# Kernel tuning notes

Measured on AMD Instinct MI355X. Metric: run time of the kernel, lower is better.

## Reference

```python
import jax, jax.numpy as jnp
import numpy as np

N_NODES = 10000
N_EDGES = 640000
STATE_DIM = 128
ACTION_DIM = 10000
K = 3  # Chebyshev order
H1, H2, H3 = 60, 30, 1
CONCAT_DIM = N_NODES + 3  # 10003


def setup_inputs() -> dict:
    key = jax.random.key(0)
    ks = jax.random.split(key, 16)
    inp = {
        "substrate_features": jax.random.normal(ks[0], (N_NODES, STATE_DIM), jnp.float32),
        "edge_index": jax.random.randint(ks[1], (2, N_EDGES), 0, N_NODES, jnp.int64),
        "v_CPU_request": jax.random.uniform(ks[2], (1,), jnp.float32),
        "v_BW_demand": jax.random.uniform(ks[3], (1,), jnp.float32),
        "pending_v_nodes": jax.random.uniform(ks[4], (1,), jnp.float32),
        # ChebConv weights: [K, in, out] (PyG stores one Linear per hop)
        "W1": jax.random.normal(ks[5], (K, STATE_DIM, H1), jnp.float32) / np.sqrt(STATE_DIM),
        "b1": jnp.zeros((H1,), jnp.float32),
        "W2": jax.random.normal(ks[6], (K, H1, H2), jnp.float32) / np.sqrt(H1),
        "b2": jnp.zeros((H2,), jnp.float32),
        "W3": jax.random.normal(ks[7], (K, H2, H3), jnp.float32) / np.sqrt(H2),
        "b3": jnp.zeros((H3,), jnp.float32),
        # actor / critic heads
        "Wa": jax.random.normal(ks[8], (ACTION_DIM, CONCAT_DIM), jnp.float32) / np.sqrt(CONCAT_DIM),
        "ba": jnp.zeros((ACTION_DIM,), jnp.float32),
        "Wc": jax.random.normal(ks[9], (1, CONCAT_DIM), jnp.float32) / np.sqrt(CONCAT_DIM),
        "bc": jnp.zeros((1,), jnp.float32),
    }
    return inp


def _edge_norm(edge_index, n_nodes):
    # PyG ChebConv sym normalization with lambda_max=2: L_hat = -D^-1/2 A D^-1/2 (diag = 0)
    src, dst = edge_index[0], edge_index[1]
    deg = jax.ops.segment_sum(jnp.ones_like(src, jnp.float32), dst, num_segments=n_nodes)
    dinv = jnp.where(deg > 0, 1.0 / jnp.sqrt(deg), 0.0)
    w = -dinv[src] * dinv[dst]  # [E]
    return src, dst, w


def _lap_matvec(x, src, dst, w, n_nodes):
    # y[i] = sum_{e: dst[e]=i} w[e] * x[src[e]]
    return jax.ops.segment_sum(w[:, None] * x[src], dst, num_segments=n_nodes)


def _cheb_conv(x, src, dst, w, n_nodes, W, b):
    # T0 = x; T1 = L_hat x; T2 = 2 L_hat T1 - T0
    Tx0 = x
    out = Tx0 @ W[0]
    Tx1 = _lap_matvec(Tx0, src, dst, w, n_nodes)
    out = out + Tx1 @ W[1]
    for k in range(2, W.shape[0]):
        Tx2 = 2.0 * _lap_matvec(Tx1, src, dst, w, n_nodes) - Tx0
        out = out + Tx2 @ W[k]
        Tx0, Tx1 = Tx1, Tx2
    return out + b


def reference(substrate_features, edge_index, v_CPU_request, v_BW_demand,
              pending_v_nodes, W1, b1, W2, b2, W3, b3, Wa, ba, Wc, bc):
    n = substrate_features.shape[0]
    src, dst, w = _edge_norm(edge_index, n)
    h = jnp.tanh(_cheb_conv(substrate_features, src, dst, w, n, W1, b1))
    h = jnp.tanh(_cheb_conv(h, src, dst, w, n, W2, b2))
    h = jnp.tanh(_cheb_conv(h, src, dst, w, n, W3, b3))  # [N, 1]
    gcn_embedding = h.reshape(1, n)  # squeeze last dim -> row vector [1, N]
    state = jnp.concatenate(
        [gcn_embedding, v_CPU_request[None, :], v_BW_demand[None, :],
         pending_v_nodes[None, :]], axis=1)  # [1, N+3]
    logits = state @ Wa.T + ba   # [1, action_dim]
    values = state @ Wc.T + bc   # [1, 1]
    return logits, values
```

## Files before the change

kernel.cpp:

```cpp
#include <hip/hip_runtime.h>
#include <hip/hip_bf16.h>

#define NN 10000
#define NE 640000
#define SD 128
#define CONCAT 10003
#define ACT 10000
#define MAXDEG 256
#define GB 2500
#define HB 2512

typedef unsigned int u32;
typedef unsigned short u16;
typedef u16 u16x8 __attribute__((ext_vector_type(8)));
typedef float f32x4 __attribute__((ext_vector_type(4)));

__device__ __forceinline__ float bf2f_bits(u16 u) {
    return __uint_as_float(((u32)u) << 16);
}
__device__ __forceinline__ float loadF(const void* base, long idx, int bf) {
    if (bf) return bf2f_bits(((const u16*)base)[idx]);
    return ((const float*)base)[idx];
}
__device__ __forceinline__ int loadI(const void* base, long idx, int i64) {
    if (i64) return (int)((const long long*)base)[idx];
    return ((const int*)base)[idx];
}

__global__ void __launch_bounds__(256) k_prep(
    const void* __restrict__ x_in, const void* __restrict__ W1,
    const void* __restrict__ Wa, const void* __restrict__ edge,
    int* __restrict__ flags, int* __restrict__ cnt,
    float* __restrict__ P0, float* __restrict__ P1, float* __restrict__ P2) {
    __shared__ int sbf;
    const int tid = threadIdx.x, gid = blockIdx.x;
    const int gtid = gid * 256 + tid;
    const int lane = tid & 63;
    const int wid = gid * 4 + (tid >> 6);

    if (tid == 0) {
        const u32* w = (const u32*)Wa;
        int c = 0;
        for (int j = 0; j < 256; ++j) {
            u32 lo = w[j] & 0xFFFFu;
            int ex = (int)((lo >> 7) & 0xFF);
            if (ex >= 100 && ex <= 140) c++;
        }
        sbf = (c >= 128) ? 1 : 0;
        if (gid == 0) {
            const int* e32 = (const int*)edge;
            int cnt64 = 0;
            for (int e = 0; e < 64; ++e) {
                int lo = e32[2 * e], hi = e32[2 * e + 1];
                if (hi == 0 && lo >= 0 && lo < NN) cnt64++;
            }
            flags[0] = (cnt64 >= 56) ? 1 : 0;
            flags[1] = sbf;
        }
    }
    __syncthreads();
    const int bf = sbf;

    for (int i = gtid; i < NN; i += GB * 256) cnt[i] = 0;

    int o = lane < 60 ? lane : 59;
    for (int r = wid; r < NN; r += GB * 4) {
        float xa, xb;
        if (bf) {
            u32 wbits = ((const u32*)x_in)[(long)r * 64 + lane];
            xa = bf2f_bits((u16)(wbits & 0xFFFFu));
            xb = bf2f_bits((u16)(wbits >> 16));
        } else {
            const float* xp = (const float*)x_in + (long)r * SD + 2 * lane;
            xa = xp[0];
            xb = xp[1];
        }
        float a0 = 0.f, a1 = 0.f, a2 = 0.f;
        for (int j2 = 0; j2 < 64; ++j2) {
            float xe = __shfl(xa, j2);
            float xo = __shfl(xb, j2);
            long je = (long)(2 * j2) * 60 + o;
            long jo = (long)(2 * j2 + 1) * 60 + o;
            a0 += xe * loadF(W1, 0 * SD * 60 + je, bf) + xo * loadF(W1, 0 * SD * 60 + jo, bf);
            a1 += xe * loadF(W1, 1 * SD * 60 + je, bf) + xo * loadF(W1, 1 * SD * 60 + jo, bf);
            a2 += xe * loadF(W1, 2 * SD * 60 + je, bf) + xo * loadF(W1, 2 * SD * 60 + jo, bf);
        }
        if (lane < 60) {
            P0[(long)r * 60 + lane] = a0;
            P1[(long)r * 60 + lane] = a1;
            P2[(long)r * 60 + lane] = a2;
        }
    }
}

__global__ void __launch_bounds__(256) k_fill(
    const void* __restrict__ edge, const int* __restrict__ flags,
    int* __restrict__ cnt, int* __restrict__ cols) {
    const int i64f = flags[0];
    int e = blockIdx.x * 256 + threadIdx.x;
    for (; e < NE; e += GB * 256) {
        int s = loadI(edge, e, i64f);
        int d = loadI(edge, NE + e, i64f);
        int pos = atomicAdd(&cnt[d], 1);
        if (pos < MAXDEG) cols[(size_t)d * MAXDEG + pos] = s;
    }
}

__global__ void __launch_bounds__(256) k_s1(
    const int* __restrict__ cnt, const int* __restrict__ cols,
    float* __restrict__ wve, const float* __restrict__ P1,
    const float* __restrict__ P2, float* __restrict__ W60) {
    const int tid = threadIdx.x;
    const int lane = tid & 63;
    const int wid = blockIdx.x * 4 + (tid >> 6);
    int o = lane < 60 ? lane : 59;
    for (int r = wid; r < NN; r += GB * 4) {
        int cr = cnt[r];
        if (cr > MAXDEG) cr = MAXDEG;
        float rr = cr > 0 ? rsqrtf((float)cr) : 0.f;
        const int* cp = cols + (size_t)r * MAXDEG;
        float* wp = wve + (size_t)r * MAXDEG;
        float acc = 0.f;
        int p = 0;
        for (; p + 3 < cr; p += 4) {
            int s0 = cp[p], s1 = cp[p + 1], s2 = cp[p + 2], s3 = cp[p + 3];
            int c0 = cnt[s0], c1 = cnt[s1], c2 = cnt[s2], c3 = cnt[s3];
            float w0 = c0 > 0 ? -rsqrtf((float)c0) * rr : 0.f;
            float w1 = c1 > 0 ? -rsqrtf((float)c1) * rr : 0.f;
            float w2 = c2 > 0 ? -rsqrtf((float)c2) * rr : 0.f;
            float w3 = c3 > 0 ? -rsqrtf((float)c3) * rr : 0.f;
            acc += w0 * P2[(size_t)s0 * 60 + o] + w1 * P2[(size_t)s1 * 60 + o] +
                   w2 * P2[(size_t)s2 * 60 + o] + w3 * P2[(size_t)s3 * 60 + o];
            if (lane == 63) {
                wp[p] = w0;
                wp[p + 1] = w1;
                wp[p + 2] = w2;
                wp[p + 3] = w3;
            }
        }
        for (; p < cr; ++p) {
            int s = cp[p];
            int cs = cnt[s];
            float w = cs > 0 ? -rsqrtf((float)cs) * rr : 0.f;
            acc += w * P2[(size_t)s * 60 + o];
            if (lane == 63) wp[p] = w;
        }
        if (lane < 60)
            W60[(size_t)r * 60 + lane] = P1[(size_t)r * 60 + lane] + 2.f * acc;
    }
}

__global__ void __launch_bounds__(256) k_s2(
    const int* __restrict__ cnt, const int* __restrict__ cols,
    const float* __restrict__ wve, const float* __restrict__ P0,
    const float* __restrict__ P2, const float* __restrict__ W60,
    const void* __restrict__ W2, const void* __restrict__ b1,
    const int* __restrict__ flags, float* __restrict__ Q0,
    float* __restrict__ Q1, float* __restrict__ Q2) {
    const int bf = flags[1];
    const int tid = threadIdx.x;
    const int lane = tid & 63;
    const int wid = blockIdx.x * 4 + (tid >> 6);
    int o = lane < 60 ? lane : 59;
    int o2 = lane < 30 ? lane : 29;
    for (int r = wid; r < NN; r += GB * 4) {
        int cr = cnt[r];
        if (cr > MAXDEG) cr = MAXDEG;
        const int* cp = cols + (size_t)r * MAXDEG;
        const float* wp = wve + (size_t)r * MAXDEG;
        float acc = 0.f;
        int p = 0;
        for (; p + 3 < cr; p += 4) {
            acc += wp[p] * W60[(size_t)cp[p] * 60 + o] +
                   wp[p + 1] * W60[(size_t)cp[p + 1] * 60 + o] +
                   wp[p + 2] * W60[(size_t)cp[p + 2] * 60 + o] +
                   wp[p + 3] * W60[(size_t)cp[p + 3] * 60 + o];
        }
        for (; p < cr; ++p) acc += wp[p] * W60[(size_t)cp[p] * 60 + o];
        float h1 = tanhf(P0[(size_t)r * 60 + o] - P2[(size_t)r * 60 + o] + acc +
                         loadF(b1, o, bf));
        float q0 = 0.f, q1 = 0.f, q2 = 0.f;
        for (int j = 0; j < 60; ++j) {
            float xj = __shfl(h1, j);
            long idx = (long)j * 30 + o2;
            q0 += xj * loadF(W2, 0 * 60 * 30 + idx, bf);
            q1 += xj * loadF(W2, 1 * 60 * 30 + idx, bf);
            q2 += xj * loadF(W2, 2 * 60 * 30 + idx, bf);
        }
        if (lane < 30) {
            Q0[(size_t)r * 30 + lane] = q0;
            Q1[(size_t)r * 30 + lane] = q1;
            Q2[(size_t)r * 30 + lane] = q2;
        }
    }
}

__global__ void __launch_bounds__(256) k_s3(
    const int* __restrict__ cnt, const int* __restrict__ cols,
    const float* __restrict__ wve, const float* __restrict__ Q1,
    const float* __restrict__ Q2, float* __restrict__ W30) {
    const int tid = threadIdx.x;
    const int lane = tid & 63;
    const int wid = blockIdx.x * 4 + (tid >> 6);
    int h = lane >> 5, l = lane & 31;
    int l2 = l < 30 ? l : 29;
    for (int r = wid; r < NN; r += GB * 4) {
        int cr = cnt[r];
        if (cr > MAXDEG) cr = MAXDEG;
        const int* cp = cols + (size_t)r * MAXDEG;
        const float* wp = wve + (size_t)r * MAXDEG;
        float acc = 0.f;
        for (int p = h; p < cr; p += 2) acc += wp[p] * Q2[(size_t)cp[p] * 30 + l2];
        acc += __shfl_xor(acc, 32);
        if (lane < 30)
            W30[(size_t)r * 30 + lane] = Q1[(size_t)r * 30 + lane] + 2.f * acc;
    }
}

__global__ void __launch_bounds__(256) k_s4(
    const int* __restrict__ cnt, const int* __restrict__ cols,
    const float* __restrict__ wve, const float* __restrict__ Q0,
    const float* __restrict__ Q2, const float* __restrict__ W30,
    const void* __restrict__ W3, const void* __restrict__ b2,
    const int* __restrict__ flags, float* __restrict__ R1,
    float* __restrict__ R2, float* __restrict__ Sa) {
    const int bf = flags[1];
    const int tid = threadIdx.x;
    const int lane = tid & 63;
    const int wid = blockIdx.x * 4 + (tid >> 6);
    int h = lane >> 5, l = lane & 31;
    int l2 = l < 30 ? l : 29;
    for (int r = wid; r < NN; r += GB * 4) {
        int cr = cnt[r];
        if (cr > MAXDEG) cr = MAXDEG;
        const int* cp = cols + (size_t)r * MAXDEG;
        const float* wp = wve + (size_t)r * MAXDEG;
        float acc = 0.f;
        for (int p = h; p < cr; p += 2) acc += wp[p] * W30[(size_t)cp[p] * 30 + l2];
        acc += __shfl_xor(acc, 32);
        float r0 = 0.f, r1 = 0.f, r2 = 0.f;
        if (l < 30) {
            float h2v = tanhf(Q0[(size_t)r * 30 + l] - Q2[(size_t)r * 30 + l] + acc +
                              loadF(b2, l, bf));
            r0 = h2v * loadF(W3, 0 * 30 + l, bf);
            r1 = h2v * loadF(W3, 1 * 30 + l, bf);
            r2 = h2v * loadF(W3, 2 * 30 + l, bf);
        }
#pragma unroll
        for (int m = 16; m; m >>= 1) {
            r0 += __shfl_xor(r0, m);
            r1 += __shfl_xor(r1, m);
            r2 += __shfl_xor(r2, m);
        }
        if (lane == 0) {
            R1[r] = r1;
            R2[r] = r2;
            Sa[r] = r0 - r2;
        }
    }
}

__global__ void __launch_bounds__(256) k_s5(
    const int* __restrict__ cnt, const int* __restrict__ cols,
    const float* __restrict__ wve, const float* __restrict__ R1,
    const float* __restrict__ R2, float* __restrict__ Wv3) {
    const int tid = threadIdx.x;
    const int lane = tid & 63;
    const int wid = blockIdx.x * 4 + (tid >> 6);
    for (int r = wid; r < NN; r += GB * 4) {
        int cr = cnt[r];
        if (cr > MAXDEG) cr = MAXDEG;
        const int* cp = cols + (size_t)r * MAXDEG;
        const float* wp = wve + (size_t)r * MAXDEG;
        float acc = 0.f;
        for (int p = lane; p < cr; p += 64) acc += wp[p] * R2[cp[p]];
#pragma unroll
        for (int m = 32; m; m >>= 1) acc += __shfl_xor(acc, m);
        if (lane == 0) Wv3[r] = R1[r] + 2.f * acc;
    }
}

__global__ void __launch_bounds__(256) k_s6(
    const int* __restrict__ cnt, const int* __restrict__ cols,
    const float* __restrict__ wve, const float* __restrict__ Sa,
    const float* __restrict__ Wv3, const void* __restrict__ b3,
    const void* sc0, const void* sc1, const void* sc2,
    const int* __restrict__ flags, float* __restrict__ state) {
    const int bf = flags[1];
    const int tid = threadIdx.x;
    const int lane = tid & 63;
    const int wid = blockIdx.x * 4 + (tid >> 6);
    for (int r = wid; r < NN; r += GB * 4) {
        int cr = cnt[r];
        if (cr > MAXDEG) cr = MAXDEG;
        const int* cp = cols + (size_t)r * MAXDEG;
        const float* wp = wve + (size_t)r * MAXDEG;
        float acc = 0.f;
        for (int p = lane; p < cr; p += 64) acc += wp[p] * Wv3[cp[p]];
#pragma unroll
        for (int m = 32; m; m >>= 1) acc += __shfl_xor(acc, m);
        if (lane == 0) state[r] = tanhf(Sa[r] + acc + loadF(b3, 0, bf));
    }
    if (blockIdx.x == 0 && tid == 0) {
        state[10000] = loadF(sc0, 0, bf);
        state[10001] = loadF(sc1, 0, bf);
        state[10002] = loadF(sc2, 0, bf);
    }
}

__global__ void __launch_bounds__(256) k_heads(
    const float* __restrict__ state, const void* __restrict__ Wa,
    const void* __restrict__ ba, const void* __restrict__ Wc,
    const void* __restrict__ bc, const int* __restrict__ flags,
    void* __restrict__ out) {
    const int bf = flags[1];
    const int tid = threadIdx.x;
    const int lane = tid & 63;
    const int wid = blockIdx.x * 4 + (tid >> 6);
    for (int r = wid; r <= ACT; r += HB * 4) {
        long base = (r < ACT) ? (long)r * CONCAT : 0;
        const void* wb = (r < ACT) ? Wa : Wc;
        float acc = 0.f;
        if (bf) {
            const u16* w = (const u16*)wb + base;
            int k = (int)((16 - ((2 * base) & 15)) & 15) >> 1;
            for (int i = lane; i < k; i += 64) acc += state[i] * bf2f_bits(w[i]);
            int nv = (CONCAT - k) >> 3;
            const u16x8* wvp = (const u16x8*)(w + k);
            for (int v = lane; v < nv; v += 64) {
                u16x8 ww = wvp[v];
                int ib = k + v * 8;
#pragma unroll
                for (int j = 0; j < 8; ++j) acc += state[ib + j] * bf2f_bits(ww[j]);
            }
            for (int i = k + nv * 8 + lane; i < CONCAT; i += 64)
                acc += state[i] * bf2f_bits(w[i]);
        } else {
            const float* w = (const float*)wb + base;
            int k = (int)((16 - ((4 * base) & 15)) & 15) >> 2;
            for (int i = lane; i < k; i += 64) acc += state[i] * w[i];
            int nv = (CONCAT - k) >> 2;
            const f32x4* wvp = (const f32x4*)(w + k);
            for (int v = lane; v < nv; v += 64) {
                f32x4 ww = wvp[v];
                int ib = k + v * 4;
#pragma unroll
                for (int j = 0; j < 4; ++j) acc += state[ib + j] * ww[j];
            }
            for (int i = k + nv * 4 + lane; i < CONCAT; i += 64)
                acc += state[i] * w[i];
        }
#pragma unroll
        for (int o = 32; o > 0; o >>= 1) acc += __shfl_xor(acc, o);
        if (lane == 0) {
            float bias = (r < ACT) ? loadF(ba, r, bf) : loadF(bc, 0, bf);
            float v = acc + bias;
            if (bf) ((__hip_bfloat16*)out)[r] = __float2bfloat16(v);
            else ((float*)out)[r] = v;
        }
    }
}

extern "C" void kernel_launch(void* const* d_in, const int* in_sizes, int n_in,
                              void* d_out, int out_size, void* d_ws, size_t ws_size,
                              hipStream_t stream) {
    const void* x_in = d_in[0];
    const void* edge = d_in[1];
    const void* sc0 = d_in[2];
    const void* sc1 = d_in[3];
    const void* sc2 = d_in[4];
    const void* W1 = d_in[5];
    const void* b1 = d_in[6];
    const void* W2 = d_in[7];
    const void* b2 = d_in[8];
    const void* W3 = d_in[9];
    const void* b3 = d_in[10];
    const void* Wa = d_in[11];
    const void* ba = d_in[12];
    const void* Wc = d_in[13];
    const void* bc = d_in[14];

    char* p = (char*)d_ws;
    auto alloc = [&](size_t bytes) {
        char* r = p;
        p += (bytes + 255) & ~(size_t)255;
        return (void*)r;
    };
    int* flags = (int*)alloc(2 * 4);
    int* cnt = (int*)alloc(NN * 4);
    int* cols = (int*)alloc((size_t)NN * MAXDEG * 4);
    float* wve = (float*)alloc((size_t)NN * MAXDEG * 4);
    float* P0 = (float*)alloc((size_t)NN * 60 * 4);
    float* P1 = (float*)alloc((size_t)NN * 60 * 4);
    float* P2 = (float*)alloc((size_t)NN * 60 * 4);
    float* W60 = (float*)alloc((size_t)NN * 60 * 4);
    float* Q0 = (float*)alloc((size_t)NN * 30 * 4);
    float* Q1 = (float*)alloc((size_t)NN * 30 * 4);
    float* Q2 = (float*)alloc((size_t)NN * 30 * 4);
    float* W30 = (float*)alloc((size_t)NN * 30 * 4);
    float* R1 = (float*)alloc(NN * 4);
    float* R2 = (float*)alloc(NN * 4);
    float* Sa = (float*)alloc(NN * 4);
    float* Wv3 = (float*)alloc(NN * 4);
    float* state = (float*)alloc(CONCAT * 4);

    k_prep<<<GB, 256, 0, stream>>>(x_in, W1, Wa, edge, flags, cnt, P0, P1, P2);
    k_fill<<<GB, 256, 0, stream>>>(edge, flags, cnt, cols);
    k_s1<<<GB, 256, 0, stream>>>(cnt, cols, wve, P1, P2, W60);
    k_s2<<<GB, 256, 0, stream>>>(cnt, cols, wve, P0, P2, W60, W2, b1, flags, Q0, Q1, Q2);
    k_s3<<<GB, 256, 0, stream>>>(cnt, cols, wve, Q1, Q2, W30);
    k_s4<<<GB, 256, 0, stream>>>(cnt, cols, wve, Q0, Q2, W30, W3, b2, flags, R1, R2, Sa);
    k_s5<<<GB, 256, 0, stream>>>(cnt, cols, wve, R1, R2, Wv3);
    k_s6<<<GB, 256, 0, stream>>>(cnt, cols, wve, Sa, Wv3, b3, sc0, sc1, sc2, flags, state);
    k_heads<<<HB, 256, 0, stream>>>(state, Wa, ba, Wc, bc, flags, d_out);
}
```

Measured before the change: 351.9 us.

## Fuse prep and fill kernels via grid barrier; fuse last two hop kernels

Merges the feature projection and CSR fill kernels into one launch of 1024 blocks. A software grid barrier separates zeroing the counters from the atomic fill; it uses per-block flags that the heads kernel resets for the next call. Also fuses the final two sparse matvecs into one kernel that recomputes each neighbor's inner sum redundantly, a two-hop gather costing roughly degree-squared work per row. This removes two launches and a global intermediate, but relies on all 1024 blocks being co-resident, and the recomputation may dominate.

```diff
diff --git a/kernel.cpp b/kernel.cpp
--- a/kernel.cpp
+++ b/kernel.cpp
@@ -7,8 +7,10 @@
 #define CONCAT 10003
 #define ACT 10000
 #define MAXDEG 256
+#define GB1 1024
 #define GB 2500
 #define HB 2512
+#define MAGIC 0x5A17C0DE
 
 typedef unsigned int u32;
 typedef unsigned short u16;
@@ -27,18 +29,27 @@
     return ((const int*)base)[idx];
 }
 
-__global__ void __launch_bounds__(256) k_prep(
+__global__ void __launch_bounds__(256, 4) k_prep_fill(
     const void* __restrict__ x_in, const void* __restrict__ W1,
     const void* __restrict__ Wa, const void* __restrict__ edge,
-    int* __restrict__ flags, int* __restrict__ cnt,
-    float* __restrict__ P0, float* __restrict__ P1, float* __restrict__ P2) {
-    __shared__ int sbf;
+    int* __restrict__ flags, int* __restrict__ cnt, int* __restrict__ cols,
+    float* __restrict__ P0, float* __restrict__ P1, float* __restrict__ P2,
+    int* bar, int* bargo) {
+    __shared__ int sflags[2];
+    __shared__ int sdone;
     const int tid = threadIdx.x, gid = blockIdx.x;
     const int gtid = gid * 256 + tid;
     const int lane = tid & 63;
     const int wid = gid * 4 + (tid >> 6);
 
     if (tid == 0) {
+        const int* e32 = (const int*)edge;
+        int cnt64 = 0;
+        for (int e = 0; e < 64; ++e) {
+            int lo = e32[2 * e], hi = e32[2 * e + 1];
+            if (hi == 0 && lo >= 0 && lo < NN) cnt64++;
+        }
+        sflags[0] = (cnt64 >= 56) ? 1 : 0;
         const u32* w = (const u32*)Wa;
         int c = 0;
         for (int j = 0; j < 256; ++j) {
@@ -46,62 +57,82 @@
             int ex = (int)((lo >> 7) & 0xFF);
             if (ex >= 100 && ex <= 140) c++;
         }
-        sbf = (c >= 128) ? 1 : 0;
+        sflags[1] = (c >= 128) ? 1 : 0;
         if (gid == 0) {
-            const int* e32 = (const int*)edge;
-            int cnt64 = 0;
-            for (int e = 0; e < 64; ++e) {
-                int lo = e32[2 * e], hi = e32[2 * e + 1];
-                if (hi == 0 && lo >= 0 && lo < NN) cnt64++;
-            }
-            flags[0] = (cnt64 >= 56) ? 1 : 0;
-            flags[1] = sbf;
+            flags[0] = sflags[0];
+            flags[1] = sflags[1];
         }
     }
     __syncthreads();
-    const int bf = sbf;
-
-    for (int i = gtid; i < NN; i += GB * 256) cnt[i] = 0;
-
-    int o = lane < 60 ? lane : 59;
-    for (int r = wid; r < NN; r += GB * 4) {
-        float xa, xb;
-        if (bf) {
-            u32 wbits = ((const u32*)x_in)[(long)r * 64 + lane];
-            xa = bf2f_bits((u16)(wbits & 0xFFFFu));
-            xb = bf2f_bits((u16)(wbits >> 16));
-        } else {
-            const float* xp = (const float*)x_in + (long)r * SD + 2 * lane;
-            xa = xp[0];
-            xb = xp[1];
-        }
-        float a0 = 0.f, a1 = 0.f, a2 = 0.f;
-        for (int j2 = 0; j2 < 64; ++j2) {
-            float xe = __shfl(xa, j2);
-            float xo = __shfl(xb, j2);
-            long je = (long)(2 * j2) * 60 + o;
-            long jo = (long)(2 * j2 + 1) * 60 + o;
-            a0 += xe * loadF(W1, 0 * SD * 60 + je, bf) + xo * loadF(W1, 0 * SD * 60 + jo, bf);
-            a1 += xe * loadF(W1, 1 * SD * 60 + je, bf) + xo * loadF(W1, 1 * SD * 60 + jo, bf);
-            a2 += xe * loadF(W1, 2 * SD * 60 + je, bf) + xo * loadF(W1, 2 * SD * 60 + jo, bf);
-        }
-        if (lane < 60) {
-            P0[(long)r * 60 + lane] = a0;
-            P1[(long)r * 60 + lane] = a1;
-            P2[(long)r * 60 + lane] = a2;
-        }
-    }
-}
-
-__global__ void __launch_bounds__(256) k_fill(
-    const void* __restrict__ edge, const int* __restrict__ flags,
-    int* __restrict__ cnt, int* __restrict__ cols) {
-    const int i64f = flags[0];
-    int e = blockIdx.x * 256 + threadIdx.x;
-    for (; e < NE; e += GB * 256) {
+    const int i64f = sflags[0], bf = sflags[1];
+
+    for (int i = gtid; i < NN; i += GB1 * 256)
+        __hip_atomic_store(&cnt[i], 0, __ATOMIC_RELAXED, __HIP_MEMORY_SCOPE_AGENT);
+
+    {
+        int o = lane < 60 ? lane : 59;
+        for (int r = wid; r < NN; r += GB1 * 4) {
+            float xa, xb;
+            if (bf) {
+                u32 wbits = ((const u32*)x_in)[(long)r * 64 + lane];
+                xa = bf2f_bits((u16)(wbits & 0xFFFFu));
+                xb = bf2f_bits((u16)(wbits >> 16));
+            } else {
+                const float* xp = (const float*)x_in + (long)r * SD + 2 * lane;
+                xa = xp[0];
+                xb = xp[1];
+            }
+            float a0 = 0.f, a1 = 0.f, a2 = 0.f;
+            for (int j2 = 0; j2 < 64; ++j2) {
+                float xe = __shfl(xa, j2);
+                float xo = __shfl(xb, j2);
+                long je = (long)(2 * j2) * 60 + o;
+                long jo = (long)(2 * j2 + 1) * 60 + o;
+                a0 += xe * loadF(W1, 0 * SD * 60 + je, bf) + xo * loadF(W1, 0 * SD * 60 + jo, bf);
+                a1 += xe * loadF(W1, 1 * SD * 60 + je, bf) + xo * loadF(W1, 1 * SD * 60 + jo, bf);
+                a2 += xe * loadF(W1, 2 * SD * 60 + je, bf) + xo * loadF(W1, 2 * SD * 60 + jo, bf);
+            }
+            if (lane < 60) {
+                P0[(long)r * 60 + lane] = a0;
+                P1[(long)r * 60 + lane] = a1;
+                P2[(long)r * 60 + lane] = a2;
+            }
+        }
+    }
+
+    asm volatile("s_waitcnt vmcnt(0)" ::: "memory");
+    __syncthreads();
+    if (tid == 0)
+        __hip_atomic_store(&bar[gid], MAGIC, __ATOMIC_RELAXED, __HIP_MEMORY_SCOPE_AGENT);
+    if (gid == 0) {
+        int it = 0;
+        while (true) {
+            if (tid == 0) sdone = 1;
+            __syncthreads();
+            int ok = 1;
+            for (int b = tid; b < GB1; b += 256)
+                if (__hip_atomic_load(&bar[b], __ATOMIC_RELAXED, __HIP_MEMORY_SCOPE_AGENT) != MAGIC)
+                    ok = 0;
+            if (!ok) sdone = 0;
+            __syncthreads();
+            if (sdone != 0 || ++it > (1 << 22)) break;
+            __builtin_amdgcn_s_sleep(4);
+        }
+        if (tid == 0)
+            __hip_atomic_store(bargo, MAGIC, __ATOMIC_RELAXED, __HIP_MEMORY_SCOPE_AGENT);
+    } else if (tid == 0) {
+        int it = 0;
+        while (__hip_atomic_load(bargo, __ATOMIC_RELAXED, __HIP_MEMORY_SCOPE_AGENT) != MAGIC) {
+            if (++it > (1 << 22)) break;
+            __builtin_amdgcn_s_sleep(8);
+        }
+    }
+    __syncthreads();
+
+    for (int e = gtid; e < NE; e += GB1 * 256) {
         int s = loadI(edge, e, i64f);
         int d = loadI(edge, NE + e, i64f);
-        int pos = atomicAdd(&cnt[d], 1);
+        int pos = __hip_atomic_fetch_add(&cnt[d], 1, __ATOMIC_RELAXED, __HIP_MEMORY_SCOPE_AGENT);
         if (pos < MAXDEG) cols[(size_t)d * MAXDEG + pos] = s;
     }
 }
@@ -260,10 +291,13 @@
     }
 }
 
-__global__ void __launch_bounds__(256) k_s5(
+__global__ void __launch_bounds__(256) k_s56(
     const int* __restrict__ cnt, const int* __restrict__ cols,
-    const float* __restrict__ wve, const float* __restrict__ R1,
-    const float* __restrict__ R2, float* __restrict__ Wv3) {
+    const float* __restrict__ wve, const float* __restrict__ Sa,
+    const float* __restrict__ R1, const float* __restrict__ R2,
+    const void* __restrict__ b3, const void* sc0, const void* sc1,
+    const void* sc2, const int* __restrict__ flags, float* __restrict__ state) {
+    const int bf = flags[1];
     const int tid = threadIdx.x;
     const int lane = tid & 63;
     const int wid = blockIdx.x * 4 + (tid >> 6);
@@ -273,30 +307,22 @@
         const int* cp = cols + (size_t)r * MAXDEG;
         const float* wp = wve + (size_t)r * MAXDEG;
         float acc = 0.f;
-        for (int p = lane; p < cr; p += 64) acc += wp[p] * R2[cp[p]];
-#pragma unroll
-        for (int m = 32; m; m >>= 1) acc += __shfl_xor(acc, m);
-        if (lane == 0) Wv3[r] = R1[r] + 2.f * acc;
-    }
-}
-
-__global__ void __launch_bounds__(256) k_s6(
-    const int* __restrict__ cnt, const int* __restrict__ cols,
-    const float* __restrict__ wve, const float* __restrict__ Sa,
-    const float* __restrict__ Wv3, const void* __restrict__ b3,
-    const void* sc0, const void* sc1, const void* sc2,
-    const int* __restrict__ flags, float* __restrict__ state) {
-    const int bf = flags[1];
-    const int tid = threadIdx.x;
-    const int lane = tid & 63;
-    const int wid = blockIdx.x * 4 + (tid >> 6);
-    for (int r = wid; r < NN; r += GB * 4) {
-        int cr = cnt[r];
-        if (cr > MAXDEG) cr = MAXDEG;
-        const int* cp = cols + (size_t)r * MAXDEG;
-        const float* wp = wve + (size_t)r * MAXDEG;
-        float acc = 0.f;
-        for (int p = lane; p < cr; p += 64) acc += wp[p] * Wv3[cp[p]];
+        for (int p = lane; p < cr; p += 64) {
+            int s = cp[p];
+            float w = wp[p];
+            int cs = cnt[s];
+            if (cs > MAXDEG) cs = MAXDEG;
+            const int* cps = cols + (size_t)s * MAXDEG;
+            const float* wps = wve + (size_t)s * MAXDEG;
+            float inner = 0.f;
+            int t = 0;
+            for (; t + 3 < cs; t += 4) {
+                inner += wps[t] * R2[cps[t]] + wps[t + 1] * R2[cps[t + 1]] +
+                         wps[t + 2] * R2[cps[t + 2]] + wps[t + 3] * R2[cps[t + 3]];
+            }
+            for (; t < cs; ++t) inner += wps[t] * R2[cps[t]];
+            acc += w * (R1[s] + 2.f * inner);
+        }
 #pragma unroll
         for (int m = 32; m; m >>= 1) acc += __shfl_xor(acc, m);
         if (lane == 0) state[r] = tanhf(Sa[r] + acc + loadF(b3, 0, bf));
@@ -312,11 +338,15 @@
     const float* __restrict__ state, const void* __restrict__ Wa,
     const void* __restrict__ ba, const void* __restrict__ Wc,
     const void* __restrict__ bc, const int* __restrict__ flags,
-    void* __restrict__ out) {
+    int* bar, int* bargo, void* __restrict__ out) {
     const int bf = flags[1];
     const int tid = threadIdx.x;
     const int lane = tid & 63;
     const int wid = blockIdx.x * 4 + (tid >> 6);
+    if (tid == 0 && blockIdx.x < GB1)
+        __hip_atomic_store(&bar[blockIdx.x], 0, __ATOMIC_RELAXED, __HIP_MEMORY_SCOPE_AGENT);
+    if (tid == 0 && blockIdx.x == GB1)
+        __hip_atomic_store(bargo, 0, __ATOMIC_RELAXED, __HIP_MEMORY_SCOPE_AGENT);
     for (int r = wid; r <= ACT; r += HB * 4) {
         long base = (r < ACT) ? (long)r * CONCAT : 0;
         const void* wb = (r < ACT) ? Wa : Wc;
@@ -387,6 +417,8 @@
         return (void*)r;
     };
     int* flags = (int*)alloc(2 * 4);
+    int* bar = (int*)alloc(GB1 * 4);
+    int* bargo = (int*)alloc(4);
     int* cnt = (int*)alloc(NN * 4);
     int* cols = (int*)alloc((size_t)NN * MAXDEG * 4);
     float* wve = (float*)alloc((size_t)NN * MAXDEG * 4);
@@ -401,16 +433,14 @@
     float* R1 = (float*)alloc(NN * 4);
     float* R2 = (float*)alloc(NN * 4);
     float* Sa = (float*)alloc(NN * 4);
-    float* Wv3 = (float*)alloc(NN * 4);
     float* state = (float*)alloc(CONCAT * 4);
 
-    k_prep<<<GB, 256, 0, stream>>>(x_in, W1, Wa, edge, flags, cnt, P0, P1, P2);
-    k_fill<<<GB, 256, 0, stream>>>(edge, flags, cnt, cols);
+    k_prep_fill<<<GB1, 256, 0, stream>>>(x_in, W1, Wa, edge, flags, cnt, cols,
+                                         P0, P1, P2, bar, bargo);
     k_s1<<<GB, 256, 0, stream>>>(cnt, cols, wve, P1, P2, W60);
     k_s2<<<GB, 256, 0, stream>>>(cnt, cols, wve, P0, P2, W60, W2, b1, flags, Q0, Q1, Q2);
     k_s3<<<GB, 256, 0, stream>>>(cnt, cols, wve, Q1, Q2, W30);
     k_s4<<<GB, 256, 0, stream>>>(cnt, cols, wve, Q0, Q2, W30, W3, b2, flags, R1, R2, Sa);
-    k_s5<<<GB, 256, 0, stream>>>(cnt, cols, wve, R1, R2, Wv3);
-    k_s6<<<GB, 256, 0, stream>>>(cnt, cols, wve, Sa, Wv3, b3, sc0, sc1, sc2, flags, state);
-    k_heads<<<HB, 256, 0, stream>>>(state, Wa, ba, Wc, bc, flags, d_out);
-}
+    k_s56<<<GB, 256, 0, stream>>>(cnt, cols, wve, Sa, R1, R2, b3, sc0, sc1, sc2, flags, state);
+    k_heads<<<HB, 256, 0, stream>>>(state, Wa, ba, Wc, bc, flags, bar, bargo, d_out);
+}
```

Measured after the change: 556.4 us. 1.58x slower.

## Fuse final three Chebyshev stages into one kernel with per-node flag spin-waits

Applied to the files above, without the earlier changes.

Merges the last three sparse stages (k_s4, k_s5, k_s6) into a single kernel of 1024 blocks, each handling a chunk of 10 rows. Intermediate per-row values R1 and Sa stay in registers. R2 and Wv3 are published as 64-bit words tagged with a magic value, and consumers spin on those words instead of waiting for kernel boundaries. This removes two launches and their global-memory round trips. In exchange it relies on all blocks being co-resident, doubles the bytes of each gathered value, and adds atomic polling. The tagged buffers are reset at the end inside k_heads so the next call starts clean.

```diff
diff --git a/kernel.cpp b/kernel.cpp
--- a/kernel.cpp
+++ b/kernel.cpp
@@ -8,10 +8,14 @@
 #define ACT 10000
 #define MAXDEG 256
 #define GB 2500
+#define GB456 1024
+#define CH456 10
 #define HB 2512
+#define MAGIC64 0x5A17C0DEull
 
 typedef unsigned int u32;
 typedef unsigned short u16;
+typedef unsigned long long u64;
 typedef u16 u16x8 __attribute__((ext_vector_type(8)));
 typedef float f32x4 __attribute__((ext_vector_type(4)));
 
@@ -25,6 +29,21 @@
 __device__ __forceinline__ int loadI(const void* base, long idx, int i64) {
     if (i64) return (int)((const long long*)base)[idx];
     return ((const int*)base)[idx];
+}
+__device__ __forceinline__ float spin_load(const u64* p) {
+    u64 v;
+    int it = 0;
+    while (true) {
+        v = __hip_atomic_load(p, __ATOMIC_RELAXED, __HIP_MEMORY_SCOPE_AGENT);
+        if ((v >> 32) == MAGIC64) break;
+        if (++it > (1 << 22)) break;
+        __builtin_amdgcn_s_sleep(1);
+    }
+    return __uint_as_float((u32)v);
+}
+__device__ __forceinline__ void publish(u64* p, float x) {
+    u64 v = (MAGIC64 << 32) | (u64)__float_as_uint(x);
+    __hip_atomic_store(p, v, __ATOMIC_RELAXED, __HIP_MEMORY_SCOPE_AGENT);
 }
 
 __global__ void __launch_bounds__(256) k_prep(
@@ -217,89 +236,96 @@
     }
 }
 
-__global__ void __launch_bounds__(256) k_s4(
+__global__ void __launch_bounds__(256, 4) k_s456(
     const int* __restrict__ cnt, const int* __restrict__ cols,
     const float* __restrict__ wve, const float* __restrict__ Q0,
     const float* __restrict__ Q2, const float* __restrict__ W30,
     const void* __restrict__ W3, const void* __restrict__ b2,
-    const int* __restrict__ flags, float* __restrict__ R1,
-    float* __restrict__ R2, float* __restrict__ Sa) {
+    const void* __restrict__ b3, const void* sc0, const void* sc1,
+    const void* sc2, const int* __restrict__ flags,
+    u64* __restrict__ R2pack, u64* __restrict__ Wv3pack,
+    float* __restrict__ state) {
     const int bf = flags[1];
     const int tid = threadIdx.x;
     const int lane = tid & 63;
-    const int wid = blockIdx.x * 4 + (tid >> 6);
-    int h = lane >> 5, l = lane & 31;
-    int l2 = l < 30 ? l : 29;
-    for (int r = wid; r < NN; r += GB * 4) {
-        int cr = cnt[r];
-        if (cr > MAXDEG) cr = MAXDEG;
-        const int* cp = cols + (size_t)r * MAXDEG;
-        const float* wp = wve + (size_t)r * MAXDEG;
-        float acc = 0.f;
-        for (int p = h; p < cr; p += 2) acc += wp[p] * W30[(size_t)cp[p] * 30 + l2];
-        acc += __shfl_xor(acc, 32);
-        float r0 = 0.f, r1 = 0.f, r2 = 0.f;
-        if (l < 30) {
-            float h2v = tanhf(Q0[(size_t)r * 30 + l] - Q2[(size_t)r * 30 + l] + acc +
-                              loadF(b2, l, bf));
-            r0 = h2v * loadF(W3, 0 * 30 + l, bf);
-            r1 = h2v * loadF(W3, 1 * 30 + l, bf);
-            r2 = h2v * loadF(W3, 2 * 30 + l, bf);
-        }
-#pragma unroll
-        for (int m = 16; m; m >>= 1) {
-            r0 += __shfl_xor(r0, m);
-            r1 += __shfl_xor(r1, m);
-            r2 += __shfl_xor(r2, m);
-        }
-        if (lane == 0) {
-            R1[r] = r1;
-            R2[r] = r2;
-            Sa[r] = r0 - r2;
-        }
-    }
-}
-
-__global__ void __launch_bounds__(256) k_s5(
-    const int* __restrict__ cnt, const int* __restrict__ cols,
-    const float* __restrict__ wve, const float* __restrict__ R1,
-    const float* __restrict__ R2, float* __restrict__ Wv3) {
-    const int tid = threadIdx.x;
-    const int lane = tid & 63;
-    const int wid = blockIdx.x * 4 + (tid >> 6);
-    for (int r = wid; r < NN; r += GB * 4) {
-        int cr = cnt[r];
-        if (cr > MAXDEG) cr = MAXDEG;
-        const int* cp = cols + (size_t)r * MAXDEG;
-        const float* wp = wve + (size_t)r * MAXDEG;
-        float acc = 0.f;
-        for (int p = lane; p < cr; p += 64) acc += wp[p] * R2[cp[p]];
-#pragma unroll
-        for (int m = 32; m; m >>= 1) acc += __shfl_xor(acc, m);
-        if (lane == 0) Wv3[r] = R1[r] + 2.f * acc;
-    }
-}
-
-__global__ void __launch_bounds__(256) k_s6(
-    const int* __restrict__ cnt, const int* __restrict__ cols,
-    const float* __restrict__ wve, const float* __restrict__ Sa,
-    const float* __restrict__ Wv3, const void* __restrict__ b3,
-    const void* sc0, const void* sc1, const void* sc2,
-    const int* __restrict__ flags, float* __restrict__ state) {
-    const int bf = flags[1];
-    const int tid = threadIdx.x;
-    const int lane = tid & 63;
-    const int wid = blockIdx.x * 4 + (tid >> 6);
-    for (int r = wid; r < NN; r += GB * 4) {
-        int cr = cnt[r];
-        if (cr > MAXDEG) cr = MAXDEG;
-        const int* cp = cols + (size_t)r * MAXDEG;
-        const float* wp = wve + (size_t)r * MAXDEG;
-        float acc = 0.f;
-        for (int p = lane; p < cr; p += 64) acc += wp[p] * Wv3[cp[p]];
-#pragma unroll
-        for (int m = 32; m; m >>= 1) acc += __shfl_xor(acc, m);
-        if (lane == 0) state[r] = tanhf(Sa[r] + acc + loadF(b3, 0, bf));
+    const int wslot = tid >> 6;
+    const int rbase = blockIdx.x * CH456;
+
+    float R1reg[3], SAreg[3];
+
+    {
+        int h = lane >> 5, l = lane & 31;
+        int l2 = l < 30 ? l : 29;
+        int k = 0;
+        for (int i = wslot; i < CH456; i += 4, ++k) {
+            int r = rbase + i;
+            if (r >= NN) break;
+            int cr = cnt[r];
+            if (cr > MAXDEG) cr = MAXDEG;
+            const int* cp = cols + (size_t)r * MAXDEG;
+            const float* wp = wve + (size_t)r * MAXDEG;
+            float acc = 0.f;
+            for (int p = h; p < cr; p += 2) acc += wp[p] * W30[(size_t)cp[p] * 30 + l2];
+            acc += __shfl_xor(acc, 32);
+            float r0 = 0.f, r1 = 0.f, r2 = 0.f;
+            if (l < 30) {
+                float h2v = tanhf(Q0[(size_t)r * 30 + l] - Q2[(size_t)r * 30 + l] + acc +
+                                  loadF(b2, l, bf));
+                r0 = h2v * loadF(W3, 0 * 30 + l, bf);
+                r1 = h2v * loadF(W3, 1 * 30 + l, bf);
+                r2 = h2v * loadF(W3, 2 * 30 + l, bf);
+            }
+#pragma unroll
+            for (int m = 16; m; m >>= 1) {
+                r0 += __shfl_xor(r0, m);
+                r1 += __shfl_xor(r1, m);
+                r2 += __shfl_xor(r2, m);
+            }
+            r0 += __shfl_xor(r0, 32);
+            r1 += __shfl_xor(r1, 32);
+            r2 += __shfl_xor(r2, 32);
+            r0 *= 0.5f;
+            r1 *= 0.5f;
+            r2 *= 0.5f;
+            R1reg[k] = r1;
+            SAreg[k] = r0 - r2;
+            if (lane == 0) publish(&R2pack[r], r2);
+        }
+    }
+
+    {
+        int k = 0;
+        for (int i = wslot; i < CH456; i += 4, ++k) {
+            int r = rbase + i;
+            if (r >= NN) break;
+            int cr = cnt[r];
+            if (cr > MAXDEG) cr = MAXDEG;
+            const int* cp = cols + (size_t)r * MAXDEG;
+            const float* wp = wve + (size_t)r * MAXDEG;
+            float acc = 0.f;
+            for (int p = lane; p < cr; p += 64) acc += wp[p] * spin_load(&R2pack[cp[p]]);
+#pragma unroll
+            for (int m = 32; m; m >>= 1) acc += __shfl_xor(acc, m);
+            float wv3 = R1reg[k] + 2.f * acc;
+            if (lane == 0) publish(&Wv3pack[r], wv3);
+        }
+    }
+
+    {
+        int k = 0;
+        for (int i = wslot; i < CH456; i += 4, ++k) {
+            int r = rbase + i;
+            if (r >= NN) break;
+            int cr = cnt[r];
+            if (cr > MAXDEG) cr = MAXDEG;
+            const int* cp = cols + (size_t)r * MAXDEG;
+            const float* wp = wve + (size_t)r * MAXDEG;
+            float acc = 0.f;
+            for (int p = lane; p < cr; p += 64) acc += wp[p] * spin_load(&Wv3pack[cp[p]]);
+#pragma unroll
+            for (int m = 32; m; m >>= 1) acc += __shfl_xor(acc, m);
+            if (lane == 0) state[r] = tanhf(SAreg[k] + acc + loadF(b3, 0, bf));
+        }
     }
     if (blockIdx.x == 0 && tid == 0) {
         state[10000] = loadF(sc0, 0, bf);
@@ -312,11 +338,16 @@
     const float* __restrict__ state, const void* __restrict__ Wa,
     const void* __restrict__ ba, const void* __restrict__ Wc,
     const void* __restrict__ bc, const int* __restrict__ flags,
+    u64* __restrict__ R2pack, u64* __restrict__ Wv3pack,
     void* __restrict__ out) {
     const int bf = flags[1];
     const int tid = threadIdx.x;
     const int lane = tid & 63;
     const int wid = blockIdx.x * 4 + (tid >> 6);
+    for (int i = blockIdx.x * 256 + tid; i < NN; i += HB * 256) {
+        R2pack[i] = 0ull;
+        Wv3pack[i] = 0ull;
+    }
     for (int r = wid; r <= ACT; r += HB * 4) {
         long base = (r < ACT) ? (long)r * CONCAT : 0;
         const void* wb = (r < ACT) ? Wa : Wc;
@@ -398,10 +429,8 @@
     float* Q1 = (float*)alloc((size_t)NN * 30 * 4);
     float* Q2 = (float*)alloc((size_t)NN * 30 * 4);
     float* W30 = (float*)alloc((size_t)NN * 30 * 4);
-    float* R1 = (float*)alloc(NN * 4);
-    float* R2 = (float*)alloc(NN * 4);
-    float* Sa = (float*)alloc(NN * 4);
-    float* Wv3 = (float*)alloc(NN * 4);
+    u64* R2pack = (u64*)alloc((size_t)NN * 8);
+    u64* Wv3pack = (u64*)alloc((size_t)NN * 8);
     float* state = (float*)alloc(CONCAT * 4);
 
     k_prep<<<GB, 256, 0, stream>>>(x_in, W1, Wa, edge, flags, cnt, P0, P1, P2);
@@ -409,8 +438,7 @@
     k_s1<<<GB, 256, 0, stream>>>(cnt, cols, wve, P1, P2, W60);
     k_s2<<<GB, 256, 0, stream>>>(cnt, cols, wve, P0, P2, W60, W2, b1, flags, Q0, Q1, Q2);
     k_s3<<<GB, 256, 0, stream>>>(cnt, cols, wve, Q1, Q2, W30);
-    k_s4<<<GB, 256, 0, stream>>>(cnt, cols, wve, Q0, Q2, W30, W3, b2, flags, R1, R2, Sa);
-    k_s5<<<GB, 256, 0, stream>>>(cnt, cols, wve, R1, R2, Wv3);
-    k_s6<<<GB, 256, 0, stream>>>(cnt, cols, wve, Sa, Wv3, b3, sc0, sc1, sc2, flags, state);
-    k_heads<<<HB, 256, 0, stream>>>(state, Wa, ba, Wc, bc, flags, d_out);
-}
+    k_s456<<<GB456, 256, 0, stream>>>(cnt, cols, wve, Q0, Q2, W30, W3, b2, b3,
+                                      sc0, sc1, sc2, flags, R2pack, Wv3pack, state);
+    k_heads<<<HB, 256, 0, stream>>>(state, Wa, ba, Wc, bc, flags, R2pack, Wv3pack, d_out);
+}
```

New measurement: 408.4 us. 16.1% more time.

## Merge prep and fill kernels using CAS slot claiming with deferred buffer reset

Applied to the files above, without the earlier changes.

Fuses the feature projection and adjacency fill into one kernel by removing the need to zero the degree counter beforehand. Edges claim slots in each destination row with a CAS on tagged column entries, and the degree is tracked with a tagged 64-bit atomicMax. The cols and degree buffers are cleared at the end of the heads kernel so the next call starts clean. This saves one launch, but the fill now does a linear CAS slot scan, which is costly for rows with high degree. It also adds a large clear pass to the heads kernel and relies on the workspace being zeroed before the first call.

```diff
diff --git a/kernel.cpp b/kernel.cpp
--- a/kernel.cpp
+++ b/kernel.cpp
@@ -9,9 +9,12 @@
 #define MAXDEG 256
 #define GB 2500
 #define HB 2512
+#define CLAIM 0x40000000u
+#define DEGTAG 0xFFFFFFFFull
 
 typedef unsigned int u32;
 typedef unsigned short u16;
+typedef unsigned long long u64;
 typedef u16 u16x8 __attribute__((ext_vector_type(8)));
 typedef float f32x4 __attribute__((ext_vector_type(4)));
 
@@ -26,19 +29,35 @@
     if (i64) return (int)((const long long*)base)[idx];
     return ((const int*)base)[idx];
 }
-
-__global__ void __launch_bounds__(256) k_prep(
+__device__ __forceinline__ bool is_claimed(u32 v) {
+    return ((v >> 28) == 0x4u) && ((v & 0x0FFFFFFFu) < NN);
+}
+__device__ __forceinline__ int degOf(const u64* __restrict__ degpack, int i) {
+    u64 v = degpack[i];
+    if ((u32)(v >> 32) != (u32)DEGTAG) return 0;
+    int d = (int)(u32)v;
+    return d > MAXDEG ? MAXDEG : d;
+}
+
+__global__ void __launch_bounds__(256) k_prep_fill(
     const void* __restrict__ x_in, const void* __restrict__ W1,
     const void* __restrict__ Wa, const void* __restrict__ edge,
-    int* __restrict__ flags, int* __restrict__ cnt,
+    int* __restrict__ flags, u32* __restrict__ cols, u64* __restrict__ degpack,
     float* __restrict__ P0, float* __restrict__ P1, float* __restrict__ P2) {
-    __shared__ int sbf;
+    __shared__ int sflags[2];
     const int tid = threadIdx.x, gid = blockIdx.x;
     const int gtid = gid * 256 + tid;
     const int lane = tid & 63;
     const int wid = gid * 4 + (tid >> 6);
 
     if (tid == 0) {
+        const int* e32 = (const int*)edge;
+        int cnt64 = 0;
+        for (int e = 0; e < 64; ++e) {
+            int lo = e32[2 * e], hi = e32[2 * e + 1];
+            if (hi == 0 && lo >= 0 && lo < NN) cnt64++;
+        }
+        sflags[0] = (cnt64 >= 56) ? 1 : 0;
         const u32* w = (const u32*)Wa;
         int c = 0;
         for (int j = 0; j < 256; ++j) {
@@ -46,68 +65,65 @@
             int ex = (int)((lo >> 7) & 0xFF);
             if (ex >= 100 && ex <= 140) c++;
         }
-        sbf = (c >= 128) ? 1 : 0;
+        sflags[1] = (c >= 128) ? 1 : 0;
         if (gid == 0) {
-            const int* e32 = (const int*)edge;
-            int cnt64 = 0;
-            for (int e = 0; e < 64; ++e) {
-                int lo = e32[2 * e], hi = e32[2 * e + 1];
-                if (hi == 0 && lo >= 0 && lo < NN) cnt64++;
-            }
-            flags[0] = (cnt64 >= 56) ? 1 : 0;
-            flags[1] = sbf;
+            flags[0] = sflags[0];
+            flags[1] = sflags[1];
         }
     }
     __syncthreads();
-    const int bf = sbf;
-
-    for (int i = gtid; i < NN; i += GB * 256) cnt[i] = 0;
-
-    int o = lane < 60 ? lane : 59;
-    for (int r = wid; r < NN; r += GB * 4) {
-        float xa, xb;
-        if (bf) {
-            u32 wbits = ((const u32*)x_in)[(long)r * 64 + lane];
-            xa = bf2f_bits((u16)(wbits & 0xFFFFu));
-            xb = bf2f_bits((u16)(wbits >> 16));
-        } else {
-            const float* xp = (const float*)x_in + (long)r * SD + 2 * lane;
-            xa = xp[0];
-            xb = xp[1];
-        }
-        float a0 = 0.f, a1 = 0.f, a2 = 0.f;
-        for (int j2 = 0; j2 < 64; ++j2) {
-            float xe = __shfl(xa, j2);
-            float xo = __shfl(xb, j2);
-            long je = (long)(2 * j2) * 60 + o;
-            long jo = (long)(2 * j2 + 1) * 60 + o;
-            a0 += xe * loadF(W1, 0 * SD * 60 + je, bf) + xo * loadF(W1, 0 * SD * 60 + jo, bf);
-            a1 += xe * loadF(W1, 1 * SD * 60 + je, bf) + xo * loadF(W1, 1 * SD * 60 + jo, bf);
-            a2 += xe * loadF(W1, 2 * SD * 60 + je, bf) + xo * loadF(W1, 2 * SD * 60 + jo, bf);
-        }
-        if (lane < 60) {
-            P0[(long)r * 60 + lane] = a0;
-            P1[(long)r * 60 + lane] = a1;
-            P2[(long)r * 60 + lane] = a2;
-        }
-    }
-}
-
-__global__ void __launch_bounds__(256) k_fill(
-    const void* __restrict__ edge, const int* __restrict__ flags,
-    int* __restrict__ cnt, int* __restrict__ cols) {
-    const int i64f = flags[0];
-    int e = blockIdx.x * 256 + threadIdx.x;
-    for (; e < NE; e += GB * 256) {
+    const int i64f = sflags[0], bf = sflags[1];
+
+    {
+        int o = lane < 60 ? lane : 59;
+        for (int r = wid; r < NN; r += GB * 4) {
+            float xa, xb;
+            if (bf) {
+                u32 wbits = ((const u32*)x_in)[(long)r * 64 + lane];
+                xa = bf2f_bits((u16)(wbits & 0xFFFFu));
+                xb = bf2f_bits((u16)(wbits >> 16));
+            } else {
+                const float* xp = (const float*)x_in + (long)r * SD + 2 * lane;
+                xa = xp[0];
+                xb = xp[1];
+            }
+            float a0 = 0.f, a1 = 0.f, a2 = 0.f;
+            for (int j2 = 0; j2 < 64; ++j2) {
+                float xe = __shfl(xa, j2);
+                float xo = __shfl(xb, j2);
+                long je = (long)(2 * j2) * 60 + o;
+                long jo = (long)(2 * j2 + 1) * 60 + o;
+                a0 += xe * loadF(W1, 0 * SD * 60 + je, bf) + xo * loadF(W1, 0 * SD * 60 + jo, bf);
+                a1 += xe * loadF(W1, 1 * SD * 60 + je, bf) + xo * loadF(W1, 1 * SD * 60 + jo, bf);
+                a2 += xe * loadF(W1, 2 * SD * 60 + je, bf) + xo * loadF(W1, 2 * SD * 60 + jo, bf);
+            }
+            if (lane < 60) {
+                P0[(long)r * 60 + lane] = a0;
+                P1[(long)r * 60 + lane] = a1;
+                P2[(long)r * 60 + lane] = a2;
+            }
+        }
+    }
+
+    for (int e = gtid; e < NE; e += GB * 256) {
         int s = loadI(edge, e, i64f);
         int d = loadI(edge, NE + e, i64f);
-        int pos = atomicAdd(&cnt[d], 1);
-        if (pos < MAXDEG) cols[(size_t)d * MAXDEG + pos] = s;
+        u32* row = cols + (size_t)d * MAXDEG;
+        u32 mark = CLAIM | (u32)s;
+        for (int slot = 0; slot < MAXDEG; ++slot) {
+            u32 v = __hip_atomic_load(&row[slot], __ATOMIC_RELAXED, __HIP_MEMORY_SCOPE_AGENT);
+            if (is_claimed(v)) continue;
+            u32 got = atomicCAS(&row[slot], v, mark);
+            if (got == v) {
+                atomicMax(&degpack[d], (DEGTAG << 32) | (u64)(slot + 1));
+                break;
+            }
+        }
     }
 }
 
 __global__ void __launch_bounds__(256) k_s1(
-    const int* __restrict__ cnt, const int* __restrict__ cols,
+    const u64* __restrict__ degpack, const u32* __restrict__ cols,
     float* __restrict__ wve, const float* __restrict__ P1,
     const float* __restrict__ P2, float* __restrict__ W60) {
     const int tid = threadIdx.x;
@@ -115,16 +131,17 @@
     const int wid = blockIdx.x * 4 + (tid >> 6);
     int o = lane < 60 ? lane : 59;
     for (int r = wid; r < NN; r += GB * 4) {
-        int cr = cnt[r];
-        if (cr > MAXDEG) cr = MAXDEG;
+        int cr = degOf(degpack, r);
         float rr = cr > 0 ? rsqrtf((float)cr) : 0.f;
-        const int* cp = cols + (size_t)r * MAXDEG;
+        const u32* cp = cols + (size_t)r * MAXDEG;
         float* wp = wve + (size_t)r * MAXDEG;
         float acc = 0.f;
         int p = 0;
         for (; p + 3 < cr; p += 4) {
-            int s0 = cp[p], s1 = cp[p + 1], s2 = cp[p + 2], s3 = cp[p + 3];
-            int c0 = cnt[s0], c1 = cnt[s1], c2 = cnt[s2], c3 = cnt[s3];
+            int s0 = cp[p] & 0x0FFFFFFF, s1 = cp[p + 1] & 0x0FFFFFFF;
+            int s2 = cp[p + 2] & 0x0FFFFFFF, s3 = cp[p + 3] & 0x0FFFFFFF;
+            int c0 = degOf(degpack, s0), c1 = degOf(degpack, s1);
+            int c2 = degOf(degpack, s2), c3 = degOf(degpack, s3);
             float w0 = c0 > 0 ? -rsqrtf((float)c0) * rr : 0.f;
             float w1 = c1 > 0 ? -rsqrtf((float)c1) * rr : 0.f;
             float w2 = c2 > 0 ? -rsqrtf((float)c2) * rr : 0.f;
@@ -139,8 +156,8 @@
             }
         }
         for (; p < cr; ++p) {
-            int s = cp[p];
-            int cs = cnt[s];
+            int s = cp[p] & 0x0FFFFFFF;
+            int cs = degOf(degpack, s);
             float w = cs > 0 ? -rsqrtf((float)cs) * rr : 0.f;
             acc += w * P2[(size_t)s * 60 + o];
             if (lane == 63) wp[p] = w;
@@ -151,7 +168,7 @@
 }
 
 __global__ void __launch_bounds__(256) k_s2(
-    const int* __restrict__ cnt, const int* __restrict__ cols,
+    const u64* __restrict__ degpack, const u32* __restrict__ cols,
     const float* __restrict__ wve, const float* __restrict__ P0,
     const float* __restrict__ P2, const float* __restrict__ W60,
     const void* __restrict__ W2, const void* __restrict__ b1,
@@ -164,19 +181,18 @@
     int o = lane < 60 ? lane : 59;
     int o2 = lane < 30 ? lane : 29;
     for (int r = wid; r < NN; r += GB * 4) {
-        int cr = cnt[r];
-        if (cr > MAXDEG) cr = MAXDEG;
-        const int* cp = cols + (size_t)r * MAXDEG;
+        int cr = degOf(degpack, r);
+        const u32* cp = cols + (size_t)r * MAXDEG;
         const float* wp = wve + (size_t)r * MAXDEG;
         float acc = 0.f;
         int p = 0;
         for (; p + 3 < cr; p += 4) {
-            acc += wp[p] * W60[(size_t)cp[p] * 60 + o] +
-                   wp[p + 1] * W60[(size_t)cp[p + 1] * 60 + o] +
-                   wp[p + 2] * W60[(size_t)cp[p + 2] * 60 + o] +
-                   wp[p + 3] * W60[(size_t)cp[p + 3] * 60 + o];
-        }
-        for (; p < cr; ++p) acc += wp[p] * W60[(size_t)cp[p] * 60 + o];
+            acc += wp[p] * W60[(size_t)(cp[p] & 0x0FFFFFFF) * 60 + o] +
+                   wp[p + 1] * W60[(size_t)(cp[p + 1] & 0x0FFFFFFF) * 60 + o] +
+                   wp[p + 2] * W60[(size_t)(cp[p + 2] & 0x0FFFFFFF) * 60 + o] +
+                   wp[p + 3] * W60[(size_t)(cp[p + 3] & 0x0FFFFFFF) * 60 + o];
+        }
+        for (; p < cr; ++p) acc += wp[p] * W60[(size_t)(cp[p] & 0x0FFFFFFF) * 60 + o];
         float h1 = tanhf(P0[(size_t)r * 60 + o] - P2[(size_t)r * 60 + o] + acc +
                          loadF(b1, o, bf));
         float q0 = 0.f, q1 = 0.f, q2 = 0.f;
@@ -196,7 +212,7 @@
 }
 
 __global__ void __launch_bounds__(256) k_s3(
-    const int* __restrict__ cnt, const int* __restrict__ cols,
+    const u64* __restrict__ degpack, const u32* __restrict__ cols,
     const float* __restrict__ wve, const float* __restrict__ Q1,
     const float* __restrict__ Q2, float* __restrict__ W30) {
     const int tid = threadIdx.x;
@@ -205,12 +221,12 @@
     int h = lane >> 5, l = lane & 31;
     int l2 = l < 30 ? l : 29;
     for (int r = wid; r < NN; r += GB * 4) {
-        int cr = cnt[r];
-        if (cr > MAXDEG) cr = MAXDEG;
-        const int* cp = cols + (size_t)r * MAXDEG;
+        int cr = degOf(degpack, r);
+        const u32* cp = cols + (size_t)r * MAXDEG;
         const float* wp = wve + (size_t)r * MAXDEG;
         float acc = 0.f;
-        for (int p = h; p < cr; p += 2) acc += wp[p] * Q2[(size_t)cp[p] * 30 + l2];
+        for (int p = h; p < cr; p += 2)
+            acc += wp[p] * Q2[(size_t)(cp[p] & 0x0FFFFFFF) * 30 + l2];
         acc += __shfl_xor(acc, 32);
         if (lane < 30)
             W30[(size_t)r * 30 + lane] = Q1[(size_t)r * 30 + lane] + 2.f * acc;
@@ -218,7 +234,7 @@
 }
 
 __global__ void __launch_bounds__(256) k_s4(
-    const int* __restrict__ cnt, const int* __restrict__ cols,
+    const u64* __restrict__ degpack, const u32* __restrict__ cols,
     const float* __restrict__ wve, const float* __restrict__ Q0,
     const float* __restrict__ Q2, const float* __restrict__ W30,
     const void* __restrict__ W3, const void* __restrict__ b2,
@@ -231,12 +247,12 @@
     int h = lane >> 5, l = lane & 31;
     int l2 = l < 30 ? l : 29;
     for (int r = wid; r < NN; r += GB * 4) {
-        int cr = cnt[r];
-        if (cr > MAXDEG) cr = MAXDEG;
-        const int* cp = cols + (size_t)r * MAXDEG;
+        int cr = degOf(degpack, r);
+        const u32* cp = cols + (size_t)r * MAXDEG;
         const float* wp = wve + (size_t)r * MAXDEG;
         float acc = 0.f;
-        for (int p = h; p < cr; p += 2) acc += wp[p] * W30[(size_t)cp[p] * 30 + l2];
+        for (int p = h; p < cr; p += 2)
+            acc += wp[p] * W30[(size_t)(cp[p] & 0x0FFFFFFF) * 30 + l2];
         acc += __shfl_xor(acc, 32);
         float r0 = 0.f, r1 = 0.f, r2 = 0.f;
         if (l < 30) {
@@ -261,19 +277,18 @@
 }
 
 __global__ void __launch_bounds__(256) k_s5(
-    const int* __restrict__ cnt, const int* __restrict__ cols,
+    const u64* __restrict__ degpack, const u32* __restrict__ cols,
     const float* __restrict__ wve, const float* __restrict__ R1,
     const float* __restrict__ R2, float* __restrict__ Wv3) {
     const int tid = threadIdx.x;
     const int lane = tid & 63;
     const int wid = blockIdx.x * 4 + (tid >> 6);
     for (int r = wid; r < NN; r += GB * 4) {
-        int cr = cnt[r];
-        if (cr > MAXDEG) cr = MAXDEG;
-        const int* cp = cols + (size_t)r * MAXDEG;
+        int cr = degOf(degpack, r);
+        const u32* cp = cols + (size_t)r * MAXDEG;
         const float* wp = wve + (size_t)r * MAXDEG;
         float acc = 0.f;
-        for (int p = lane; p < cr; p += 64) acc += wp[p] * R2[cp[p]];
+        for (int p = lane; p < cr; p += 64) acc += wp[p] * R2[cp[p] & 0x0FFFFFFF];
 #pragma unroll
         for (int m = 32; m; m >>= 1) acc += __shfl_xor(acc, m);
         if (lane == 0) Wv3[r] = R1[r] + 2.f * acc;
@@ -281,7 +296,7 @@
 }
 
 __global__ void __launch_bounds__(256) k_s6(
-    const int* __restrict__ cnt, const int* __restrict__ cols,
+    const u64* __restrict__ degpack, const u32* __restrict__ cols,
     const float* __restrict__ wve, const float* __restrict__ Sa,
     const float* __restrict__ Wv3, const void* __restrict__ b3,
     const void* sc0, const void* sc1, const void* sc2,
@@ -291,12 +306,11 @@
     const int lane = tid & 63;
     const int wid = blockIdx.x * 4 + (tid >> 6);
     for (int r = wid; r < NN; r += GB * 4) {
-        int cr = cnt[r];
-        if (cr > MAXDEG) cr = MAXDEG;
-        const int* cp = cols + (size_t)r * MAXDEG;
+        int cr = degOf(degpack, r);
+        const u32* cp = cols + (size_t)r * MAXDEG;
         const float* wp = wve + (size_t)r * MAXDEG;
         float acc = 0.f;
-        for (int p = lane; p < cr; p += 64) acc += wp[p] * Wv3[cp[p]];
+        for (int p = lane; p < cr; p += 64) acc += wp[p] * Wv3[cp[p] & 0x0FFFFFFF];
 #pragma unroll
         for (int m = 32; m; m >>= 1) acc += __shfl_xor(acc, m);
         if (lane == 0) state[r] = tanhf(Sa[r] + acc + loadF(b3, 0, bf));
@@ -312,11 +326,13 @@
     const float* __restrict__ state, const void* __restrict__ Wa,
     const void* __restrict__ ba, const void* __restrict__ Wc,
     const void* __restrict__ bc, const int* __restrict__ flags,
-    void* __restrict__ out) {
+    u32* __restrict__ cols, u64* __restrict__ degpack, void* __restrict__ out) {
     const int bf = flags[1];
     const int tid = threadIdx.x;
     const int lane = tid & 63;
     const int wid = blockIdx.x * 4 + (tid >> 6);
+    for (int i = blockIdx.x * 256 + tid; i < NN * MAXDEG; i += HB * 256) cols[i] = 0u;
+    for (int i = blockIdx.x * 256 + tid; i < NN; i += HB * 256) degpack[i] = 0ull;
     for (int r = wid; r <= ACT; r += HB * 4) {
         long base = (r < ACT) ? (long)r * CONCAT : 0;
         const void* wb = (r < ACT) ? Wa : Wc;
@@ -387,8 +403,8 @@
         return (void*)r;
     };
     int* flags = (int*)alloc(2 * 4);
-    int* cnt = (int*)alloc(NN * 4);
-    int* cols = (int*)alloc((size_t)NN * MAXDEG * 4);
+    u32* cols = (u32*)alloc((size_t)NN * MAXDEG * 4);
+    u64* degpack = (u64*)alloc((size_t)NN * 8);
     float* wve = (float*)alloc((size_t)NN * MAXDEG * 4);
     float* P0 = (float*)alloc((size_t)NN * 60 * 4);
     float* P1 = (float*)alloc((size_t)NN * 60 * 4);
@@ -404,13 +420,13 @@
     float* Wv3 = (float*)alloc(NN * 4);
     float* state = (float*)alloc(CONCAT * 4);
 
-    k_prep<<<GB, 256, 0, stream>>>(x_in, W1, Wa, edge, flags, cnt, P0, P1, P2);
-    k_fill<<<GB, 256, 0, stream>>>(edge, flags, cnt, cols);
-    k_s1<<<GB, 256, 0, stream>>>(cnt, cols, wve, P1, P2, W60);
-    k_s2<<<GB, 256, 0, stream>>>(cnt, cols, wve, P0, P2, W60, W2, b1, flags, Q0, Q1, Q2);
-    k_s3<<<GB, 256, 0, stream>>>(cnt, cols, wve, Q1, Q2, W30);
-    k_s4<<<GB, 256, 0, stream>>>(cnt, cols, wve, Q0, Q2, W30, W3, b2, flags, R1, R2, Sa);
-    k_s5<<<GB, 256, 0, stream>>>(cnt, cols, wve, R1, R2, Wv3);
-    k_s6<<<GB, 256, 0, stream>>>(cnt, cols, wve, Sa, Wv3, b3, sc0, sc1, sc2, flags, state);
-    k_heads<<<HB, 256, 0, stream>>>(state, Wa, ba, Wc, bc, flags, d_out);
-}
+    k_prep_fill<<<GB, 256, 0, stream>>>(x_in, W1, Wa, edge, flags, cols, degpack,
+                                        P0, P1, P2);
+    k_s1<<<GB, 256, 0, stream>>>(degpack, cols, wve, P1, P2, W60);
+    k_s2<<<GB, 256, 0, stream>>>(degpack, cols, wve, P0, P2, W60, W2, b1, flags, Q0, Q1, Q2);
+    k_s3<<<GB, 256, 0, stream>>>(degpack, cols, wve, Q1, Q2, W30);
+    k_s4<<<GB, 256, 0, stream>>>(degpack, cols, wve, Q0, Q2, W30, W3, b2, flags, R1, R2, Sa);
+    k_s5<<<GB, 256, 0, stream>>>(degpack, cols, wve, R1, R2, Wv3);
+    k_s6<<<GB, 256, 0, stream>>>(degpack, cols, wve, Sa, Wv3, b3, sc0, sc1, sc2, flags, state);
+    k_heads<<<HB, 256, 0, stream>>>(state, Wa, ba, Wc, bc, flags, cols, degpack, d_out);
+}
```

After: 970.6 us. 2.76x slower.
